# Performance work log

Measured on AMD Instinct MI355X. Metric: run time of the kernel, lower is better.

Reference implementation:

```python
import jax, jax.numpy as jnp
import numpy as np

B, N, F_IN, H, OUT = 64, 1024, 195, 128, 64
K1, K2 = N // 2, N // 4  # ceil(0.5*N), ceil(0.5*K1)
EPS = 1e-5


def setup_inputs() -> dict:
    key = jax.random.key(0)
    ks = jax.random.split(key, 16)
    rn = lambda k, s: jax.random.normal(k, s, dtype=jnp.float32) * 0.1
    inp = {
        "input": jax.random.normal(ks[0], (B, N, F_IN), dtype=jnp.float32),
        # SAGEConv1 (195->128): lin_l (neighbors, w/ bias), lin_r (root, no bias)
        "W1l": rn(ks[1], (H, F_IN)), "b1l": jnp.zeros((H,), jnp.float32),
        "W1r": rn(ks[2], (H, F_IN)),
        # SAGPooling1 GNN = GraphConv(128->1): lin_rel (sum aggr, w/ bias), lin_root (no bias)
        "Wp1_rel": rn(ks[3], (1, H)), "bp1_rel": jnp.zeros((1,), jnp.float32),
        "Wp1_root": rn(ks[4], (1, H)),
        # SAGEConv2 (128->64)
        "W2l": rn(ks[5], (OUT, H)), "b2l": jnp.zeros((OUT,), jnp.float32),
        "W2r": rn(ks[6], (OUT, H)),
        # SAGPooling2 GNN = GraphConv(64->1)
        "Wp2_rel": rn(ks[7], (1, OUT)), "bp2_rel": jnp.zeros((1,), jnp.float32),
        "Wp2_root": rn(ks[8], (1, OUT)),
        # MLP head
        "fc1_w": rn(ks[9], (512, OUT)), "fc1_b": jnp.zeros((512,), jnp.float32),
        "bn1_g": jnp.ones((512,), jnp.float32), "bn1_b": jnp.zeros((512,), jnp.float32),
        "bn1_m": jnp.zeros((512,), jnp.float32), "bn1_v": jnp.ones((512,), jnp.float32),
        "fc2_w": rn(ks[10], (256, 512)), "fc2_b": jnp.zeros((256,), jnp.float32),
        "bn2_g": jnp.ones((256,), jnp.float32), "bn2_b": jnp.zeros((256,), jnp.float32),
        "bn2_m": jnp.zeros((256,), jnp.float32), "bn2_v": jnp.ones((256,), jnp.float32),
        "fc3_w": rn(ks[11], (2, 256)), "fc3_b": jnp.zeros((2,), jnp.float32),
    }
    return inp


def _corr_adj(x):
    # Pearson corrcoef over rows of x [B,N,F] -> boolean adjacency [B,N,N] (corr > 0.5)
    xc = x - x.mean(axis=-1, keepdims=True)
    cov = jnp.einsum("bnf,bmf->bnm", xc, xc)
    d = jnp.sqrt(jnp.clip(jnp.einsum("bnnf->bn", cov[..., None] * 0 + 0) + jnp.diagonal(cov, axis1=1, axis2=2), 1e-12))
    corr = cov / (d[:, :, None] * d[:, None, :])
    return (corr > 0.5).astype(x.dtype)  # symmetric, includes self-loops


def _sage(x, A, Wl, bl, Wr):
    # PyG SAGEConv: lin_l(mean_{j in N(i)} x_j) + lin_r(x_i)
    deg = A.sum(axis=-1, keepdims=True)
    agg = jnp.einsum("bnm,bmf->bnf", A, x) / jnp.maximum(deg, 1.0)
    return jnp.einsum("bnf,hf->bnh", agg, Wl) + bl + jnp.einsum("bnf,hf->bnh", x, Wr)


def _sagpool(x, A, Wrel, brel, Wroot, k):
    # score via GraphConv (sum aggr): lin_rel(sum_j x_j) + lin_root(x_i)
    agg = jnp.einsum("bnm,bmf->bnf", A, x)
    score = (jnp.einsum("bnf,of->bno", agg, Wrel) + brel
             + jnp.einsum("bnf,of->bno", x, Wroot))[..., 0]  # [B,N]
    top_s, idx = jax.lax.top_k(score, k)  # per-graph top-k nodes
    x_new = jnp.take_along_axis(x, idx[:, :, None], axis=1) * jnp.tanh(top_s)[:, :, None]
    A_new = jnp.take_along_axis(A, idx[:, :, None], axis=1)
    A_new = jnp.take_along_axis(A_new, idx[:, None, :], axis=2)
    return x_new, A_new


def _bn_eval(x, g, b, m, v):
    return g * (x - m) * jax.lax.rsqrt(v + EPS) + b


def reference(input, W1l, b1l, W1r, Wp1_rel, bp1_rel, Wp1_root,
              W2l, b2l, W2r, Wp2_rel, bp2_rel, Wp2_root,
              fc1_w, fc1_b, bn1_g, bn1_b, bn1_m, bn1_v,
              fc2_w, fc2_b, bn2_g, bn2_b, bn2_m, bn2_v,
              fc3_w, fc3_b):
    A = _corr_adj(input)                                   # [B,N,N]
    x = jax.nn.relu(_sage(input, A, W1l, b1l, W1r))        # [B,N,128]
    x, A = _sagpool(x, A, Wp1_rel, bp1_rel, Wp1_root, K1)  # [B,K1,128]
    x = jax.nn.relu(_sage(x, A, W2l, b2l, W2r))            # [B,K1,64]
    x, A = _sagpool(x, A, Wp2_rel, bp2_rel, Wp2_root, K2)  # [B,K2,64]
    x = x.mean(axis=1)                                     # global mean pool -> [B,64]
    x = _bn_eval(jax.nn.relu(x @ fc1_w.T + fc1_b), bn1_g, bn1_b, bn1_m, bn1_v)
    x = _bn_eval(jax.nn.relu(x @ fc2_w.T + fc2_b), bn2_g, bn2_b, bn2_m, bn2_v)
    x = x @ fc3_w.T + fc3_b
    return jax.nn.softmax(x, axis=1)
```

## Files before the change

kernel.cpp:

```cpp
#include <hip/hip_runtime.h>
#include <hip/hip_fp8.h>
#include <cstdint>


typedef __bf16 bf16x8 __attribute__((ext_vector_type(8)));
typedef float  floatx4 __attribute__((ext_vector_type(4)));

#define MFMA_BF16(a, b, c) __builtin_amdgcn_mfma_f32_16x16x32_bf16((a), (b), (c), 0, 0, 0)
#define MFMA_FP8(a, b, c)  __builtin_amdgcn_mfma_f32_16x16x32_fp8_fp8((a), (b), (c), 0, 0, 0)

static constexpr int BATCH = 64, NNODE = 1024, FIN = 195, FPAD = 224;
static constexpr int HD = 128, OD = 64, KP1 = 512, KP2 = 256;

static constexpr size_t OFF_GHI   = 0;
static constexpr size_t OFF_GLO   = 8388608;
static constexpr size_t OFF_A1B   = 16777216;
static constexpr size_t OFF_YR2   = 18874368;
static constexpr size_t OFF_X2    = 35651584;
static constexpr size_t OFF_XHI   = 0;
static constexpr size_t OFF_XLO   = 29360128;
static constexpr size_t OFF_ABITS = 58720256;
static constexpr size_t OFF_X1    = 67108864;
static constexpr size_t OFF_P1    = 100663296;
static constexpr size_t OFF_Q1    = OFF_P1 + 262144;
static constexpr size_t OFF_IDX1  = OFF_Q1 + 262144;
static constexpr size_t OFF_GATE1 = OFF_IDX1 + 131072;
static constexpr size_t OFF_P2    = OFF_GATE1 + 131072;
static constexpr size_t OFF_Q2    = OFF_P2 + 131072;
static constexpr size_t OFF_W1HI  = OFF_Q2 + 131072;
static constexpr size_t OFF_W1LO  = OFF_W1HI + 114688;
static constexpr size_t OFF_W2HI  = OFF_W1LO + 114688;
static constexpr size_t OFF_W2LO  = OFF_W2HI + 32768;
static constexpr size_t OFF_XHAT  = 102760448;
static constexpr size_t OFF_YR1   = 102760448 + 16777216;

static __device__ __forceinline__ unsigned char to_fp8(float v) {
  __hip_fp8_e4m3 q(v);
  return *(unsigned char*)&q;
}

__global__ __launch_bounds__(256) void prep_pack_kernel(
    const float* __restrict__ x, __bf16* __restrict__ xhi,
    __bf16* __restrict__ xlo, unsigned char* __restrict__ xhat8,
    const float* __restrict__ W1l, const float* __restrict__ W1r,
    __bf16* __restrict__ hi1, __bf16* __restrict__ lo1,
    const float* __restrict__ W2l, const float* __restrict__ W2r,
    __bf16* __restrict__ hi2, __bf16* __restrict__ lo2) {
  int bid = blockIdx.x;
  if (bid < 16384) {
    int row  = bid * 4 + (threadIdx.x >> 6);
    int lane = threadIdx.x & 63;
    const float* xr = x + (long)row * FIN;
    int k0 = lane * 4;
    float v[4];
#pragma unroll
    for (int i = 0; i < 4; ++i) v[i] = (k0 + i < FIN) ? xr[k0 + i] : 0.f;
    float s = v[0] + v[1] + v[2] + v[3];
#pragma unroll
    for (int o = 32; o; o >>= 1) s += __shfl_xor(s, o);
    float mean = s * (1.f / (float)FIN);
    float c[4], ss = 0.f;
#pragma unroll
    for (int i = 0; i < 4; ++i) {
      c[i] = (k0 + i < FIN) ? (v[i] - mean) : 0.f;
      ss += c[i] * c[i];
    }
#pragma unroll
    for (int o = 32; o; o >>= 1) ss += __shfl_xor(ss, o);
    float inv = rsqrtf(fmaxf(ss, 1e-12f));
    if (k0 < FPAD) {
      __bf16 hi4[4], lo4[4];
      unsigned char h8[4];
#pragma unroll
      for (int i = 0; i < 4; ++i) {
        float xv = (k0 + i < FIN) ? v[i] : 0.f;
        __bf16 h = (__bf16)xv;
        hi4[i] = h;
        lo4[i] = (__bf16)(xv - (float)h);
        h8[i] = to_fp8(c[i] * inv);
      }
      long base = (long)row * FPAD + k0;
      *(uint2*)&xhi[base] = *(const uint2*)hi4;
      *(uint2*)&xlo[base] = *(const uint2*)lo4;
      *(unsigned int*)&xhat8[base] = *(const unsigned int*)h8;
    }
  } else if (bid < 16384 + 224) {
    int idx = (bid - 16384) * 256 + threadIdx.x;
    int h = idx / FPAD, k = idx % FPAD;
    float v = 0.f;
    if (k < FIN) v = (h < HD) ? W1l[h * FIN + k] : W1r[(h - HD) * FIN + k];
    __bf16 a = (__bf16)v;
    hi1[idx] = a;
    lo1[idx] = (__bf16)(v - (float)a);
  } else {
    int idx = (bid - 16384 - 224) * 256 + threadIdx.x;
    int h = idx / HD, k = idx % HD;
    float v = (h < OD) ? W2l[h * HD + k] : W2r[(h - OD) * HD + k];
    __bf16 a = (__bf16)v;
    hi2[idx] = a;
    lo2[idx] = (__bf16)(v - (float)a);
  }
}

static constexpr int CKB = 48;
__global__ __launch_bounds__(256) void corr_kernel(
    const unsigned char* __restrict__ xhat8, unsigned short* __restrict__ Abits) {
  __shared__ __align__(16) unsigned char sI[128 * CKB];
  __shared__ __align__(16) unsigned char sJ[128 * CKB];
  int bid = blockIdx.x;
  int xcd = bid & 7;
  int m = bid >> 3;
  int b = xcd + ((m & 7) << 3);
  int rem = m >> 3, bi = 0;
  while (rem >= 8 - bi) { rem -= 8 - bi; ++bi; }
  int bj = bi + rem;
  int i0 = bi * 128, j0 = bj * 128;
  const unsigned char* Xb = xhat8 + (long)b * NNODE * FPAD;
  int lane = threadIdx.x & 63, wave = threadIdx.x >> 6;
  int wi = (wave >> 1) * 64, wj = (wave & 1) * 64;
  int lr = lane & 15, lk8 = (lane >> 4) * 8;
  int strow = threadIdx.x & 127;
  int sbuf = threadIdx.x >> 7;
  floatx4 zero = {0.f, 0.f, 0.f, 0.f};
  floatx4 acc[4][4];
#pragma unroll
  for (int i = 0; i < 4; ++i)
#pragma unroll
    for (int j = 0; j < 4; ++j) acc[i][j] = zero;
  for (int kk = 0; kk < 7; ++kk) {
    int k0 = kk * 32;
    __syncthreads();
    {
      unsigned char* dst = (sbuf ? sJ : sI) + strow * CKB;
      const unsigned char* src = Xb + (long)((sbuf ? j0 : i0) + strow) * FPAD + k0;
      *(uint4*)(dst)      = *(const uint4*)(src);
      *(uint4*)(dst + 16) = *(const uint4*)(src + 16);
    }
    __syncthreads();
    long long af[4], bf[4];
#pragma unroll
    for (int t = 0; t < 4; ++t) {
      af[t] = *(const long long*)&sI[(wi + t * 16 + lr) * CKB + lk8];
      bf[t] = *(const long long*)&sJ[(wj + t * 16 + lr) * CKB + lk8];
    }
#pragma unroll
    for (int ti = 0; ti < 4; ++ti)
#pragma unroll
      for (int tj = 0; tj < 4; ++tj)
        acc[ti][tj] = MFMA_FP8(af[ti], bf[tj], acc[ti][tj]);
  }
#pragma unroll
  for (int ti = 0; ti < 4; ++ti)
#pragma unroll
    for (int tj = 0; tj < 4; ++tj) {
      floatx4 a = acc[ti][tj];
      unsigned long long m0 = __ballot(a[0] > 0.5f);
      unsigned long long m1 = __ballot(a[1] > 0.5f);
      unsigned long long m2 = __ballot(a[2] > 0.5f);
      unsigned long long m3 = __ballot(a[3] > 0.5f);
      if (lane < 16) {
        unsigned long long mm = (lane & 2) ? ((lane & 1) ? m3 : m2)
                                           : ((lane & 1) ? m1 : m0);
        unsigned short piece = (unsigned short)(mm >> ((lane >> 2) * 16));
        int grow = i0 + wi + ti * 16 + lane;
        int gcol = (j0 + wj + tj * 16) >> 4;
        Abits[((long)b * NNODE + grow) * 64 + gcol] = piece;
      }
    }
}

template <int K, int NCOL>
__global__ __launch_bounds__(256, 2) void gemm_split_kernel(
    const __bf16* __restrict__ Ahi, const __bf16* __restrict__ Alo,
    const __bf16* __restrict__ Bhi, const __bf16* __restrict__ Blo,
    float* __restrict__ C, int mblocks,
    unsigned long long* __restrict__ A64, int ntrans) {
  constexpr int ldc = NCOL * 128;
  int bid = blockIdx.x;
  if (bid >= mblocks * NCOL) {
    int t = bid - mblocks * NCOL;
    if (t >= ntrans) return;
    int b = t / 28, pi = t % 28;
    int rem = pi, rb = 1;
    while (rem >= rb) { rem -= rb; ++rb; }
    int cb = rem;
    int wave = threadIdx.x >> 6, lane = threadIdx.x & 63;
    int dr = rb * 2 + (wave >> 1);
    int dc = cb * 2 + (wave & 1);
    long base = (long)b * NNODE;
    unsigned long long xv = A64[(base + dc * 64 + lane) * 16 + dr];
    const unsigned long long M1  = 0x5555555555555555ULL;
    const unsigned long long M2  = 0x3333333333333333ULL;
    const unsigned long long M4  = 0x0F0F0F0F0F0F0F0FULL;
    const unsigned long long M8  = 0x00FF00FF00FF00FFULL;
    const unsigned long long M16 = 0x0000FFFF0000FFFFULL;
    const unsigned long long M32 = 0x00000000FFFFFFFFULL;
#define TSTEP(Kk, M)                                                      \
    {                                                                     \
      unsigned long long y = __shfl_xor(xv, Kk);                          \
      xv = ((lane & Kk) == 0) ? ((xv & (M)) | ((y & (M)) << Kk))          \
                              : ((xv & ~(M)) | ((y & ~(M)) >> Kk));       \
    }
    TSTEP(1, M1) TSTEP(2, M2) TSTEP(4, M4) TSTEP(8, M8) TSTEP(16, M16) TSTEP(32, M32)
#undef TSTEP
    A64[(base + dr * 64 + lane) * 16 + dc] = xv;
    return;
  }
  int mrow, col;
  if (NCOL == 2) {
    int xcd = bid & 7;
    int q = bid >> 3;
    col = q & 1;
    mrow = (xcd << 6) + (q >> 1);
  } else {
    mrow = bid;
    col = 0;
  }
  long row0 = (long)mrow * 128;
  int col0 = col * 128;
  int lane = threadIdx.x & 63, wave = threadIdx.x >> 6;
  int wi = (wave >> 1) * 64, wj = (wave & 1) * 64;
  int lr = lane & 15, lk = (lane >> 4) * 8;
  const __bf16* pAh = Ahi + (row0 + wi + lr) * (long)K + lk;
  const __bf16* pAl = Alo + (row0 + wi + lr) * (long)K + lk;
  const __bf16* pBh = Bhi + (long)(col0 + wj + lr) * K + lk;
  const __bf16* pBl = Blo + (long)(col0 + wj + lr) * K + lk;
  floatx4 zero = {0.f, 0.f, 0.f, 0.f};
  floatx4 acc[4][4];
#pragma unroll
  for (int i = 0; i < 4; ++i)
#pragma unroll
    for (int j = 0; j < 4; ++j) acc[i][j] = zero;
#pragma unroll
  for (int kk = 0; kk < (K >> 5); ++kk) {
    int k0 = kk * 32;
    bf16x8 ah[4], al[4], bh[4], bl[4];
#pragma unroll
    for (int t = 0; t < 4; ++t) {
      ah[t] = *(const bf16x8*)(pAh + (long)t * 16 * K + k0);
      al[t] = *(const bf16x8*)(pAl + (long)t * 16 * K + k0);
      bh[t] = *(const bf16x8*)(pBh + (long)t * 16 * K + k0);
      bl[t] = *(const bf16x8*)(pBl + (long)t * 16 * K + k0);
    }
#pragma unroll
    for (int tj = 0; tj < 4; ++tj)
#pragma unroll
      for (int ti = 0; ti < 4; ++ti) {
        acc[ti][tj] = MFMA_BF16(ah[ti], bh[tj], acc[ti][tj]);
        acc[ti][tj] = MFMA_BF16(ah[ti], bl[tj], acc[ti][tj]);
        acc[ti][tj] = MFMA_BF16(al[ti], bh[tj], acc[ti][tj]);
      }
  }
#pragma unroll
  for (int ti = 0; ti < 4; ++ti)
#pragma unroll
    for (int tj = 0; tj < 4; ++tj)
#pragma unroll
      for (int rr = 0; rr < 4; ++rr) {
        long grow = row0 + wi + ti * 16 + (lane >> 4) * 4 + rr;
        int gcol = col0 + wj + tj * 16 + (lane & 15);
        C[grow * ldc + gcol] = acc[ti][tj][rr];
      }
}

__global__ __launch_bounds__(256) void sage1_kernel(
    const unsigned int* __restrict__ Abits32, const float* __restrict__ YR1,
    const float* __restrict__ b1l, const float* __restrict__ Wrel,
    const float* __restrict__ Wroot, float* __restrict__ x1,
    float* __restrict__ p1, float* __restrict__ q1) {
  int g = threadIdx.x >> 5;
  int lane = threadIdx.x & 31;
  int node = blockIdx.x * 8 + g;
  int b = node >> 10, nloc = node & 1023;
  __shared__ int list[8][1024];
  __shared__ int s_deg[8];
  {
    unsigned int word = Abits32[(long)node * 32 + lane];
    int cnt = __popc(word);
    int off = cnt;
#pragma unroll
    for (int o = 1; o < 32; o <<= 1) {
      int v = __shfl_up(off, o, 32);
      if (lane >= o) off += v;
    }
    off -= cnt;
    if (lane == 31) s_deg[g] = off + cnt;
    int basei = lane * 32;
    while (word) {
      int t = __ffs(word) - 1;
      word &= word - 1;
      list[g][off++] = basei + t;
    }
  }
  __syncthreads();
  int deg = s_deg[g];
  const float4* Y4 = (const float4*)(YR1 + (long)(b << 10) * 256);
  float4 a4 = {0.f, 0.f, 0.f, 0.f};
  for (int d = 0; d < deg; ++d) {
    float4 y = Y4[(long)list[g][d] * 64 + lane];
    a4.x += y.x; a4.y += y.y; a4.z += y.z; a4.w += y.w;
  }
  float4 R = Y4[(long)nloc * 64 + 32 + lane];
  float inv = 1.f / (float)(deg < 1 ? 1 : deg);
  float4 bl = ((const float4*)b1l)[lane];
  float4 v;
  v.x = fmaxf(a4.x * inv + bl.x + R.x, 0.f);
  v.y = fmaxf(a4.y * inv + bl.y + R.y, 0.f);
  v.z = fmaxf(a4.z * inv + bl.z + R.z, 0.f);
  v.w = fmaxf(a4.w * inv + bl.w + R.w, 0.f);
  ((float4*)x1)[(long)node * 32 + lane] = v;
  float4 wr = ((const float4*)Wrel)[lane];
  float4 wq = ((const float4*)Wroot)[lane];
  float pv = v.x * wr.x + v.y * wr.y + v.z * wr.z + v.w * wr.w;
  float qv = v.x * wq.x + v.y * wq.y + v.z * wq.z + v.w * wq.w;
#pragma unroll
  for (int o = 16; o; o >>= 1) {
    pv += __shfl_xor(pv, o, 32);
    qv += __shfl_xor(qv, o, 32);
  }
  if (lane == 0) { p1[node] = pv; q1[node] = qv; }
}

__global__ void scoretopk_kernel(const unsigned int* __restrict__ bits32,
                                 const float* __restrict__ p,
                                 const float* __restrict__ q,
                                 const float* __restrict__ brel,
                                 int* __restrict__ idx_out,
                                 float* __restrict__ gate_out,
                                 int nwords, int rpb_shift, int k) {
  int b = blockIdx.x, tid = threadIdx.x;
  int row = (b << rpb_shift) + tid;
  const unsigned int* wptr = bits32 + (long)row * nwords;
  const float* pb = p + ((long)b << rpb_shift);
  float s = q[row] + brel[0];
  for (int w = 0; w < nwords; ++w) {
    unsigned int word = wptr[w];
    while (word) {
      int t = __ffs(word) - 1;
      word &= word - 1;
      s += pb[w * 32 + t];
    }
  }
  unsigned int fb = __float_as_uint(s);
  unsigned int key = (fb & 0x80000000u) ? ~fb : (fb | 0x80000000u);
  __shared__ int hist[256];
  __shared__ unsigned int sh_prefix;
  __shared__ int sh_target, cnt_gt, cnt_eq, outpos;
  if (tid == 0) { sh_prefix = 0; sh_target = k; cnt_gt = 0; cnt_eq = 0; outpos = 0; }
  for (int shift = 24; shift >= 0; shift -= 8) {
    if (tid < 256) hist[tid] = 0;
    __syncthreads();
    unsigned int prefix = sh_prefix;
    bool inset = (shift == 24) || ((key >> (shift + 8)) == (prefix >> (shift + 8)));
    if (inset) atomicAdd(&hist[(key >> shift) & 255], 1);
    __syncthreads();
    if (tid < 64) {
      int lane = tid;
      int bb0 = hist[255 - 4 * lane];
      int bb1 = hist[254 - 4 * lane];
      int bb2 = hist[253 - 4 * lane];
      int bb3 = hist[252 - 4 * lane];
      int c0 = bb0, c1 = c0 + bb1, c2 = c1 + bb2, c3 = c2 + bb3;
      int incl = c3;
#pragma unroll
      for (int o = 1; o < 64; o <<= 1) {
        int v = __shfl_up(incl, o);
        if (lane >= o) incl += v;
      }
      int excl = incl - c3;
      int target = sh_target;
      int cum[4] = {excl + c0, excl + c1, excl + c2, excl + c3};
      int prev = excl;
#pragma unroll
      for (int i = 0; i < 4; ++i) {
        if (cum[i] >= target && prev < target) {
          int bin = 255 - (4 * lane + i);
          sh_prefix = prefix | ((unsigned int)bin << shift);
          sh_target = target - prev;
        }
        prev = cum[i];
      }
    }
    __syncthreads();
  }
  unsigned int T = sh_prefix;
  if (key > T) atomicAdd(&cnt_gt, 1);
  __syncthreads();
  int E = k - cnt_gt;
  bool sel = (key > T);
  if (!sel && key == T) sel = (atomicAdd(&cnt_eq, 1) < E);
  if (sel) {
    int posn = atomicAdd(&outpos, 1);
    idx_out[b * k + posn] = tid;
    gate_out[b * k + posn] = tanhf(s);
  }
}

__global__ __launch_bounds__(256) void gather_kernel(
    const float* __restrict__ x1, const int* __restrict__ idx,
    const float* __restrict__ gate, __bf16* __restrict__ ghi,
    __bf16* __restrict__ glo, const unsigned int* __restrict__ Abits32,
    unsigned long long* __restrict__ A1bits) {
  int bid = blockIdx.x;
  if (bid < 16384) {
    long e = (long)bid * 256 + threadIdx.x;
    int h = (int)(e & 127);
    int i = (int)((e >> 7) & 511);
    int b = (int)(e >> 16);
    int srow = idx[(b << 9) + i];
    float v = x1[((long)(b << 10) + srow) * 128 + h] * gate[(b << 9) + i];
    __bf16 a = (__bf16)v;
    ghi[e] = a;
    glo[e] = (__bf16)(v - (float)a);
  } else {
    int gi = (bid - 16384) * 4 + (threadIdx.x >> 6);
    int lane = threadIdx.x & 63;
    int b = gi >> 9;
    int srow = idx[gi];
    const unsigned int* src = Abits32 + ((long)(b << 10) + srow) * 32;
    const int* idxb = idx + (b << 9);
#pragma unroll
    for (int t = 0; t < 8; ++t) {
      int cj = idxb[t * 64 + lane];
      int bit = (src[cj >> 5] >> (cj & 31)) & 1;
      unsigned long long m = __ballot(bit);
      if (lane == 0) A1bits[(long)gi * 8 + t] = m;
    }
  }
}

__global__ __launch_bounds__(256) void sage2_kernel(
    const unsigned int* __restrict__ A1b32, const float* __restrict__ YR2,
    const float* __restrict__ b2l, const float* __restrict__ Wrel,
    const float* __restrict__ Wroot, float* __restrict__ x2,
    float* __restrict__ p2, float* __restrict__ q2) {
  int g = threadIdx.x >> 4;
  int lane = threadIdx.x & 15;
  int row = blockIdx.x * 16 + g;
  int b = row >> 9, iloc = row & 511;
  __shared__ int list[16][512];
  __shared__ int s_deg[16];
  {
    unsigned int word = A1b32[(long)row * 16 + lane];
    int cnt = __popc(word);
    int off = cnt;
#pragma unroll
    for (int o = 1; o < 16; o <<= 1) {
      int v = __shfl_up(off, o, 16);
      if (lane >= o) off += v;
    }
    off -= cnt;
    if (lane == 15) s_deg[g] = off + cnt;
    int basei = lane * 32;
    while (word) {
      int t = __ffs(word) - 1;
      word &= word - 1;
      list[g][off++] = basei + t;
    }
  }
  __syncthreads();
  int deg = s_deg[g];
  const float4* Y4 = (const float4*)(YR2 + (long)(b << 9) * 128);
  float4 a4 = {0.f, 0.f, 0.f, 0.f};
  for (int d = 0; d < deg; ++d) {
    float4 y = Y4[(long)list[g][d] * 32 + lane];
    a4.x += y.x; a4.y += y.y; a4.z += y.z; a4.w += y.w;
  }
  float4 R = Y4[(long)iloc * 32 + 16 + lane];
  float inv = 1.f / (float)(deg < 1 ? 1 : deg);
  float4 bl = ((const float4*)b2l)[lane];
  float4 v;
  v.x = fmaxf(a4.x * inv + bl.x + R.x, 0.f);
  v.y = fmaxf(a4.y * inv + bl.y + R.y, 0.f);
  v.z = fmaxf(a4.z * inv + bl.z + R.z, 0.f);
  v.w = fmaxf(a4.w * inv + bl.w + R.w, 0.f);
  ((float4*)x2)[(long)row * 16 + lane] = v;
  float4 wr = ((const float4*)Wrel)[lane];
  float4 wq = ((const float4*)Wroot)[lane];
  float pv = v.x * wr.x + v.y * wr.y + v.z * wr.z + v.w * wr.w;
  float qv = v.x * wq.x + v.y * wq.y + v.z * wq.z + v.w * wq.w;
#pragma unroll
  for (int o = 8; o; o >>= 1) {
    pv += __shfl_xor(pv, o, 16);
    qv += __shfl_xor(qv, o, 16);
  }
  if (lane == 0) { p2[row] = pv; q2[row] = qv; }
}

__global__ __launch_bounds__(512) void scoretopk_head_kernel(
    const unsigned int* __restrict__ A1b32, const float* __restrict__ p2,
    const float* __restrict__ q2, const float* __restrict__ brel,
    const float* __restrict__ x2, const float* __restrict__ fc1_w,
    const float* __restrict__ fc1_b, const float* __restrict__ g1,
    const float* __restrict__ bb1, const float* __restrict__ m1,
    const float* __restrict__ v1, const float* __restrict__ fc2_w,
    const float* __restrict__ fc2_b, const float* __restrict__ g2,
    const float* __restrict__ bb2, const float* __restrict__ m2,
    const float* __restrict__ v2, const float* __restrict__ fc3_w,
    const float* __restrict__ fc3_b, float* __restrict__ out) {
  int b = blockIdx.x, tid = threadIdx.x;
  int row = (b << 9) + tid;
  const unsigned int* wptr = A1b32 + (long)row * 16;
  const float* pb = p2 + ((long)b << 9);
  float s = q2[row] + brel[0];
  for (int w = 0; w < 16; ++w) {
    unsigned int word = wptr[w];
    while (word) {
      int t = __ffs(word) - 1;
      word &= word - 1;
      s += pb[w * 32 + t];
    }
  }
  constexpr int k = KP2;
  unsigned int fb = __float_as_uint(s);
  unsigned int key = (fb & 0x80000000u) ? ~fb : (fb | 0x80000000u);
  __shared__ int hist[256];
  __shared__ int idx2s[256];
  __shared__ float gate2s[256];
  __shared__ unsigned int sh_prefix;
  __shared__ int sh_target, cnt_gt, cnt_eq, outpos;
  if (tid == 0) { sh_prefix = 0; sh_target = k; cnt_gt = 0; cnt_eq = 0; outpos = 0; }
  for (int shift = 24; shift >= 0; shift -= 8) {
    if (tid < 256) hist[tid] = 0;
    __syncthreads();
    unsigned int prefix = sh_prefix;
    bool inset = (shift == 24) || ((key >> (shift + 8)) == (prefix >> (shift + 8)));
    if (inset) atomicAdd(&hist[(key >> shift) & 255], 1);
    __syncthreads();
    if (tid < 64) {
      int lane = tid;
      int bb0 = hist[255 - 4 * lane];
      int bb1 = hist[254 - 4 * lane];
      int bb2 = hist[253 - 4 * lane];
      int bb3 = hist[252 - 4 * lane];
      int c0 = bb0, c1 = c0 + bb1, c2 = c1 + bb2, c3 = c2 + bb3;
      int incl = c3;
#pragma unroll
      for (int o = 1; o < 64; o <<= 1) {
        int v = __shfl_up(incl, o);
        if (lane >= o) incl += v;
      }
      int excl = incl - c3;
      int target = sh_target;
      int cum[4] = {excl + c0, excl + c1, excl + c2, excl + c3};
      int prev = excl;
#pragma unroll
      for (int i = 0; i < 4; ++i) {
        if (cum[i] >= target && prev < target) {
          int bin = 255 - (4 * lane + i);
          sh_prefix = prefix | ((unsigned int)bin << shift);
          sh_target = target - prev;
        }
        prev = cum[i];
      }
    }
    __syncthreads();
  }
  unsigned int T = sh_prefix;
  if (key > T) atomicAdd(&cnt_gt, 1);
  __syncthreads();
  int E = k - cnt_gt;
  bool sel = (key > T);
  if (!sel && key == T) sel = (atomicAdd(&cnt_eq, 1) < E);
  if (sel) {
    int posn = atomicAdd(&outpos, 1);
    idx2s[posn] = tid;
    gate2s[posn] = tanhf(s);
  }
  __syncthreads();
  __shared__ float part[8][64];
  __shared__ float pooled[64];
  __shared__ float h1[512];
  __shared__ float h2[256];
  __shared__ float zz[2];
  int h = tid & 63, grp = tid >> 6;
  float sp = 0.f;
  for (int i = grp * 32; i < grp * 32 + 32; ++i) {
    int si = idx2s[i];
    sp += x2[((long)(b << 9) + si) * 64 + h] * gate2s[i];
  }
  part[grp][h] = sp;
  __syncthreads();
  if (tid < 64) {
    float t = 0.f;
#pragma unroll
    for (int g = 0; g < 8; ++g) t += part[g][tid];
    pooled[tid] = t * (1.f / 256.f);
  }
  __syncthreads();
  {
    float z = fc1_b[tid];
    for (int j = 0; j < 64; ++j) z += pooled[j] * fc1_w[tid * 64 + j];
    z = fmaxf(z, 0.f);
    h1[tid] = g1[tid] * (z - m1[tid]) * rsqrtf(v1[tid] + 1e-5f) + bb1[tid];
  }
  __syncthreads();
  if (tid < 256) {
    float z = fc2_b[tid];
    for (int j = 0; j < 512; ++j) z += h1[j] * fc2_w[tid * 512 + j];
    z = fmaxf(z, 0.f);
    h2[tid] = g2[tid] * (z - m2[tid]) * rsqrtf(v2[tid] + 1e-5f) + bb2[tid];
  }
  __syncthreads();
  if (tid < 2) {
    float z = fc3_b[tid];
    for (int j = 0; j < 256; ++j) z += h2[j] * fc3_w[tid * 256 + j];
    zz[tid] = z;
  }
  __syncthreads();
  if (tid == 0) {
    float mx = fmaxf(zz[0], zz[1]);
    float e0 = expf(zz[0] - mx), e1 = expf(zz[1] - mx);
    float inv = 1.f / (e0 + e1);
    out[b * 2 + 0] = e0 * inv;
    out[b * 2 + 1] = e1 * inv;
  }
}

extern "C" void kernel_launch(void* const* d_in, const int* in_sizes, int n_in,
                              void* d_out, int out_size, void* d_ws, size_t ws_size,
                              hipStream_t stream) {
  (void)in_sizes; (void)n_in; (void)out_size; (void)ws_size;
  const float* input   = (const float*)d_in[0];
  const float* W1l     = (const float*)d_in[1];
  const float* b1l     = (const float*)d_in[2];
  const float* W1r     = (const float*)d_in[3];
  const float* Wp1_rel = (const float*)d_in[4];
  const float* bp1_rel = (const float*)d_in[5];
  const float* Wp1_root= (const float*)d_in[6];
  const float* W2l     = (const float*)d_in[7];
  const float* b2l     = (const float*)d_in[8];
  const float* W2r     = (const float*)d_in[9];
  const float* Wp2_rel = (const float*)d_in[10];
  const float* bp2_rel = (const float*)d_in[11];
  const float* Wp2_root= (const float*)d_in[12];
  const float* fc1_w   = (const float*)d_in[13];
  const float* fc1_b   = (const float*)d_in[14];
  const float* bn1_g   = (const float*)d_in[15];
  const float* bn1_b   = (const float*)d_in[16];
  const float* bn1_m   = (const float*)d_in[17];
  const float* bn1_v   = (const float*)d_in[18];
  const float* fc2_w   = (const float*)d_in[19];
  const float* fc2_b   = (const float*)d_in[20];
  const float* bn2_g   = (const float*)d_in[21];
  const float* bn2_b   = (const float*)d_in[22];
  const float* bn2_m   = (const float*)d_in[23];
  const float* bn2_v   = (const float*)d_in[24];
  const float* fc3_w   = (const float*)d_in[25];
  const float* fc3_b   = (const float*)d_in[26];

  char* ws = (char*)d_ws;
  __bf16* xhi   = (__bf16*)(ws + OFF_XHI);
  __bf16* xlo   = (__bf16*)(ws + OFF_XLO);
  unsigned char* xhat8 = (unsigned char*)(ws + OFF_XHAT);
  unsigned short* Abits = (unsigned short*)(ws + OFF_ABITS);
  const unsigned int* Abits32 = (const unsigned int*)(ws + OFF_ABITS);
  unsigned long long* A64 = (unsigned long long*)(ws + OFF_ABITS);
  float* YR1    = (float*)(ws + OFF_YR1);
  float* x1     = (float*)(ws + OFF_X1);
  float* p1     = (float*)(ws + OFF_P1);
  float* q1     = (float*)(ws + OFF_Q1);
  int*   idx1   = (int*)(ws + OFF_IDX1);
  float* gate1  = (float*)(ws + OFF_GATE1);
  float* p2     = (float*)(ws + OFF_P2);
  float* q2     = (float*)(ws + OFF_Q2);
  __bf16* w1hi  = (__bf16*)(ws + OFF_W1HI);
  __bf16* w1lo  = (__bf16*)(ws + OFF_W1LO);
  __bf16* w2hi  = (__bf16*)(ws + OFF_W2HI);
  __bf16* w2lo  = (__bf16*)(ws + OFF_W2LO);
  __bf16* ghi   = (__bf16*)(ws + OFF_GHI);
  __bf16* glo   = (__bf16*)(ws + OFF_GLO);
  unsigned long long* A1bits = (unsigned long long*)(ws + OFF_A1B);
  const unsigned int* A1b32  = (const unsigned int*)(ws + OFF_A1B);
  float* YR2    = (float*)(ws + OFF_YR2);
  float* x2     = (float*)(ws + OFF_X2);
  float* out    = (float*)d_out;

  prep_pack_kernel<<<16672, 256, 0, stream>>>(input, xhi, xlo, xhat8,
                                              W1l, W1r, w1hi, w1lo,
                                              W2l, W2r, w2hi, w2lo);
  corr_kernel<<<2304, 256, 0, stream>>>(xhat8, Abits);
  gemm_split_kernel<224, 2><<<1024 + 1792, 256, 0, stream>>>(
      xhi, xlo, w1hi, w1lo, YR1, 512, A64, 1792);
  sage1_kernel<<<8192, 256, 0, stream>>>(Abits32, YR1, b1l, Wp1_rel, Wp1_root, x1, p1, q1);
  scoretopk_kernel<<<64, 1024, 0, stream>>>(Abits32, p1, q1, bp1_rel, idx1, gate1,
                                            32, 10, KP1);
  gather_kernel<<<24576, 256, 0, stream>>>(x1, idx1, gate1, ghi, glo, Abits32, A1bits);
  gemm_split_kernel<128, 1><<<256, 256, 0, stream>>>(
      ghi, glo, w2hi, w2lo, YR2, 256, nullptr, 0);
  sage2_kernel<<<2048, 256, 0, stream>>>(A1b32, YR2, b2l, Wp2_rel, Wp2_root, x2, p2, q2);
  scoretopk_head_kernel<<<64, 512, 0, stream>>>(A1b32, p2, q2, bp2_rel, x2,
                                                fc1_w, fc1_b, bn1_g, bn1_b, bn1_m, bn1_v,
                                                fc2_w, fc2_b, bn2_g, bn2_b, bn2_m, bn2_v,
                                                fc3_w, fc3_b, out);
}
```

Measured before the change: 350.6 us.

## Stage split-bf16 GEMM operand tiles in LDS via global_load_lds

The split hi/lo bf16 GEMM now stages the A and B tiles for each k-step in shared memory using direct global-to-LDS 16-byte loads. Each wave then reads its MFMA fragments from LDS, so one block-wide load replaces duplicated per-wave global loads. Launch bounds are raised to 3 blocks per SM to improve occupancy. The cost is two barriers per k-step with no double buffering, and the 64-byte LDS row stride may cause bank conflicts. The fully unrolled k-loop is also dropped.

```diff
diff --git a/kernel.cpp b/kernel.cpp
--- a/kernel.cpp
+++ b/kernel.cpp
@@ -8,6 +8,12 @@
 
 #define MFMA_BF16(a, b, c) __builtin_amdgcn_mfma_f32_16x16x32_bf16((a), (b), (c), 0, 0, 0)
 #define MFMA_FP8(a, b, c)  __builtin_amdgcn_mfma_f32_16x16x32_fp8_fp8((a), (b), (c), 0, 0, 0)
+
+typedef __attribute__((address_space(1))) const void as1_cvoid;
+typedef __attribute__((address_space(3))) void as3_void;
+static __device__ __forceinline__ void gl16(const void* g, void* l) {
+  __builtin_amdgcn_global_load_lds((as1_cvoid*)g, (as3_void*)l, 16, 0, 0);
+}
 
 static constexpr int BATCH = 64, NNODE = 1024, FIN = 195, FPAD = 224;
 static constexpr int HD = 128, OD = 64, KP1 = 512, KP2 = 256;
@@ -170,7 +176,7 @@
 }
 
 template <int K, int NCOL>
-__global__ __launch_bounds__(256, 2) void gemm_split_kernel(
+__global__ __launch_bounds__(256, 3) void gemm_split_kernel(
     const __bf16* __restrict__ Ahi, const __bf16* __restrict__ Alo,
     const __bf16* __restrict__ Bhi, const __bf16* __restrict__ Blo,
     float* __restrict__ C, int mblocks,
@@ -216,40 +222,57 @@
     mrow = bid;
     col = 0;
   }
+  __shared__ __align__(16) __bf16 sAh[128 * 32];
+  __shared__ __align__(16) __bf16 sAl[128 * 32];
+  __shared__ __align__(16) __bf16 sBh[128 * 32];
+  __shared__ __align__(16) __bf16 sBl[128 * 32];
   long row0 = (long)mrow * 128;
   int col0 = col * 128;
-  int lane = threadIdx.x & 63, wave = threadIdx.x >> 6;
+  int t = threadIdx.x;
+  int lane = t & 63, wave = t >> 6;
   int wi = (wave >> 1) * 64, wj = (wave & 1) * 64;
-  int lr = lane & 15, lk = (lane >> 4) * 8;
-  const __bf16* pAh = Ahi + (row0 + wi + lr) * (long)K + lk;
-  const __bf16* pAl = Alo + (row0 + wi + lr) * (long)K + lk;
-  const __bf16* pBh = Bhi + (long)(col0 + wj + lr) * K + lk;
-  const __bf16* pBl = Blo + (long)(col0 + wj + lr) * K + lk;
+  int lr = lane & 15, lk2 = (lane >> 4) * 16;
+  int sr = t >> 2, sc = (t & 3) * 8;
+  const char* gA0 = (const char*)(Ahi + (row0 + sr) * (long)K + sc);
+  const char* gA1 = (const char*)(Alo + (row0 + sr) * (long)K + sc);
+  const char* gB0 = (const char*)(Bhi + (long)(col0 + sr) * K + sc);
+  const char* gB1 = (const char*)(Blo + (long)(col0 + sr) * K + sc);
+  constexpr long rstep = 64L * K * 2;
+  char* lAh = (char*)sAh + (wave << 10);
+  char* lAl = (char*)sAl + (wave << 10);
+  char* lBh = (char*)sBh + (wave << 10);
+  char* lBl = (char*)sBl + (wave << 10);
   floatx4 zero = {0.f, 0.f, 0.f, 0.f};
   floatx4 acc[4][4];
 #pragma unroll
   for (int i = 0; i < 4; ++i)
 #pragma unroll
     for (int j = 0; j < 4; ++j) acc[i][j] = zero;
-#pragma unroll
   for (int kk = 0; kk < (K >> 5); ++kk) {
-    int k0 = kk * 32;
-    bf16x8 ah[4], al[4], bh[4], bl[4];
-#pragma unroll
-    for (int t = 0; t < 4; ++t) {
-      ah[t] = *(const bf16x8*)(pAh + (long)t * 16 * K + k0);
-      al[t] = *(const bf16x8*)(pAl + (long)t * 16 * K + k0);
-      bh[t] = *(const bf16x8*)(pBh + (long)t * 16 * K + k0);
-      bl[t] = *(const bf16x8*)(pBl + (long)t * 16 * K + k0);
-    }
-#pragma unroll
-    for (int tj = 0; tj < 4; ++tj)
-#pragma unroll
-      for (int ti = 0; ti < 4; ++ti) {
-        acc[ti][tj] = MFMA_BF16(ah[ti], bh[tj], acc[ti][tj]);
-        acc[ti][tj] = MFMA_BF16(ah[ti], bl[tj], acc[ti][tj]);
-        acc[ti][tj] = MFMA_BF16(al[ti], bh[tj], acc[ti][tj]);
-      }
+    __syncthreads();
+    gl16(gA0, lAh); gl16(gA0 + rstep, lAh + 4096);
+    gl16(gA1, lAl); gl16(gA1 + rstep, lAl + 4096);
+    gl16(gB0, lBh); gl16(gB0 + rstep, lBh + 4096);
+    gl16(gB1, lBl); gl16(gB1 + rstep, lBl + 4096);
+    gA0 += 64; gA1 += 64; gB0 += 64; gB1 += 64;
+    __syncthreads();
+    bf16x8 bh[4], bl[4];
+#pragma unroll
+    for (int tj = 0; tj < 4; ++tj) {
+      bh[tj] = *(const bf16x8*)((const char*)sBh + (wj + tj * 16 + lr) * 64 + lk2);
+      bl[tj] = *(const bf16x8*)((const char*)sBl + (wj + tj * 16 + lr) * 64 + lk2);
+    }
+#pragma unroll
+    for (int ti = 0; ti < 4; ++ti) {
+      bf16x8 ah = *(const bf16x8*)((const char*)sAh + (wi + ti * 16 + lr) * 64 + lk2);
+      bf16x8 al = *(const bf16x8*)((const char*)sAl + (wi + ti * 16 + lr) * 64 + lk2);
+#pragma unroll
+      for (int tj = 0; tj < 4; ++tj) acc[ti][tj] = MFMA_BF16(ah, bh[tj], acc[ti][tj]);
+#pragma unroll
+      for (int tj = 0; tj < 4; ++tj) acc[ti][tj] = MFMA_BF16(ah, bl[tj], acc[ti][tj]);
+#pragma unroll
+      for (int tj = 0; tj < 4; ++tj) acc[ti][tj] = MFMA_BF16(al, bh[tj], acc[ti][tj]);
+    }
   }
 #pragma unroll
   for (int ti = 0; ti < 4; ++ti)
```

After: 337.8 us. 1.04x faster.
